# Performance work log

Hardware: AMD Instinct MI355X
Metric: run time of the kernel (lower is better)

The kernel has to match this reference:

```python
import jax, jax.numpy as jnp
import numpy as np

TOP_K = 8


def setup_inputs() -> dict:
    key = jax.random.key(0)
    k1, k2, k3 = jax.random.split(key, 3)
    tokens, hidden, experts = 32768, 2048, 64
    hidden_states = jax.random.normal(k1, (tokens, hidden), dtype=jnp.float32)
    weight = jax.random.normal(k2, (experts, hidden), dtype=jnp.float32) * 0.02
    bias = jax.random.normal(k3, (experts,), dtype=jnp.float32) * 0.02
    return {"hidden_states": hidden_states, "weight": weight, "bias": bias}


def reference(hidden_states, weight, bias):
    # router logits: [tokens, experts]
    logits = jnp.einsum('th,eh->te', hidden_states, weight) + bias
    top_vals, top_idx = jax.lax.top_k(logits, TOP_K)            # [tokens, k]
    top_probs = jax.nn.softmax(top_vals, axis=-1)               # softmax over selected k
    rows = jnp.arange(logits.shape[0])[:, None]                  # [tokens, 1]
    scores = jnp.zeros_like(logits).at[rows, top_idx].set(top_probs)
    return scores, top_idx
```

## Files before the change

### kernel.cpp

```cpp
#include <hip/hip_runtime.h>
#include <math.h>

typedef _Float16 half8 __attribute__((ext_vector_type(8)));
typedef _Float16 half4 __attribute__((ext_vector_type(4)));
typedef float    f32x4 __attribute__((ext_vector_type(4)));

#define TOKENS  32768
#define HIDDEN  2048
#define EXPERTS 64
#define TOPK    8
#define BKW     64
#define NWIN    (HIDDEN / BKW)
#define LDH     72

__global__ __launch_bounds__(256, 1)
void router_mfma(const float* __restrict__ A,
                 const float* __restrict__ W,
                 const float* __restrict__ bias,
                 float* __restrict__ out) {
    __shared__ __align__(16) _Float16 hsm[4 * 64 * LDH];
    _Float16* Ahs = hsm;
    _Float16* Als = hsm + 64 * LDH;
    _Float16* Whs = hsm + 2 * 64 * LDH;
    _Float16* Wls = hsm + 3 * 64 * LDH;

    const int tid = threadIdx.x;
    const int w   = tid >> 6;
    const int l   = tid & 63;
    const int g   = blockIdx.x;

    const int s_tok = tid >> 4;
    const int s_c   = tid & 15;
    const int we = tid >> 2;
    const int wc = tid & 3;

    const float* Abase = A + (size_t)g * 64 * HIDDEN;
    const float* WBase = W + (size_t)we * HIDDEN;

    f32x4 acc[4];
    #pragma unroll
    for (int n = 0; n < 4; ++n) acc[n] = (f32x4){0.f, 0.f, 0.f, 0.f};

    float4 ar0, ar1, ar2, ar3;
    float4 wr0, wr1, wr2, wr3;

    #define LOADA(win) do {                                                  \
        const float* p_ = Abase + (size_t)(win) * BKW + s_c * 4;             \
        ar0 = *(const float4*)(p_ + (size_t)(s_tok     ) * HIDDEN);          \
        ar1 = *(const float4*)(p_ + (size_t)(s_tok + 16) * HIDDEN);          \
        ar2 = *(const float4*)(p_ + (size_t)(s_tok + 32) * HIDDEN);          \
        ar3 = *(const float4*)(p_ + (size_t)(s_tok + 48) * HIDDEN);          \
    } while (0)

    #define LOADW(win) do {                                                  \
        const float* q_ = WBase + (size_t)(win) * BKW + wc * 8;              \
        wr0 = *(const float4*)(q_);                                          \
        wr1 = *(const float4*)(q_ + 4);                                      \
        wr2 = *(const float4*)(q_ + 32);                                     \
        wr3 = *(const float4*)(q_ + 36);                                     \
    } while (0)

    #define SPLIT4(HS, LS, v, OFF) do {                                      \
        _Float16 h0_ = (_Float16)(v).x, h1_ = (_Float16)(v).y;               \
        _Float16 h2_ = (_Float16)(v).z, h3_ = (_Float16)(v).w;               \
        half4 hh_ = {h0_, h1_, h2_, h3_};                                    \
        half4 ll_ = {(_Float16)((v).x - (float)h0_),                         \
                     (_Float16)((v).y - (float)h1_),                         \
                     (_Float16)((v).z - (float)h2_),                         \
                     (_Float16)((v).w - (float)h3_)};                        \
        *(half4*)(&(HS)[(OFF)]) = hh_;                                       \
        *(half4*)(&(LS)[(OFF)]) = ll_;                                       \
    } while (0)

    #define STAGE() do {                                                     \
        SPLIT4(Ahs, Als, ar0, (s_tok     ) * LDH + s_c * 4);                 \
        SPLIT4(Ahs, Als, ar1, (s_tok + 16) * LDH + s_c * 4);                 \
        SPLIT4(Ahs, Als, ar2, (s_tok + 32) * LDH + s_c * 4);                 \
        SPLIT4(Ahs, Als, ar3, (s_tok + 48) * LDH + s_c * 4);                 \
        SPLIT4(Whs, Wls, wr0, we * LDH + wc * 8);                            \
        SPLIT4(Whs, Wls, wr1, we * LDH + wc * 8 + 4);                        \
        SPLIT4(Whs, Wls, wr2, we * LDH + wc * 8 + 32);                       \
        SPLIT4(Whs, Wls, wr3, we * LDH + wc * 8 + 36);                       \
    } while (0)

    LOADA(0);
    LOADW(0);

    #pragma unroll 1
    for (int win = 0; win < NWIN; ++win) {
        __syncthreads();
        STAGE();
        __syncthreads();

        if (win + 1 < NWIN) {
            LOADA(win + 1);
            LOADW(win + 1);
        }

        #pragma unroll
        for (int ks = 0; ks < 2; ++ks) {
            const int ko = ks * 32 + (l >> 4) * 8;
            half8 ahi = *(const half8*)(&Ahs[(w * 16 + (l & 15)) * LDH + ko]);
            half8 alo = *(const half8*)(&Als[(w * 16 + (l & 15)) * LDH + ko]);
            #pragma unroll
            for (int n = 0; n < 4; ++n) {
                half8 bh = *(const half8*)(&Whs[(n * 16 + (l & 15)) * LDH + ko]);
                half8 bl = *(const half8*)(&Wls[(n * 16 + (l & 15)) * LDH + ko]);
                acc[n] = __builtin_amdgcn_mfma_f32_16x16x32_f16(ahi, bh, acc[n], 0, 0, 0);
                acc[n] = __builtin_amdgcn_mfma_f32_16x16x32_f16(ahi, bl, acc[n], 0, 0, 0);
                acc[n] = __builtin_amdgcn_mfma_f32_16x16x32_f16(alo, bh, acc[n], 0, 0, 0);
            }
        }
    }
    #undef LOADA
    #undef LOADW
    #undef SPLIT4
    #undef STAGE

    __syncthreads();
    float* lg = (float*)hsm;
    float* sc = (float*)hsm + 64 * 68;

    #pragma unroll
    for (int n = 0; n < 4; ++n) {
        float b = bias[n * 16 + (l & 15)];
        #pragma unroll
        for (int q = 0; q < 4; ++q) {
            int trow = w * 16 + (l >> 4) * 4 + q;
            lg[trow * 68 + n * 16 + (l & 15)] = acc[n][q] + b;
        }
    }
    for (int i = tid; i < 64 * 65; i += 256) sc[i] = 0.f;
    __syncthreads();

    if (tid < 64) {
        const int t = tid;
        float v[64];
        #pragma unroll
        for (int e = 0; e < 64; ++e) v[e] = lg[t * 68 + e];

        float tvals[TOPK]; int tix[TOPK]; float probs[TOPK];
        unsigned long long chosen = 0ull;
        #pragma unroll
        for (int j = 0; j < TOPK; ++j) {
            float best = -INFINITY; int bi = 0;
            #pragma unroll
            for (int e = 0; e < 64; ++e) {
                bool ok = ((chosen >> e) & 1ull) == 0ull;
                if (ok && v[e] > best) { best = v[e]; bi = e; }
            }
            chosen |= (1ull << bi);
            tvals[j] = best; tix[j] = bi;
        }
        float m = tvals[0];
        float ssum = 0.f;
        #pragma unroll
        for (int j = 0; j < TOPK; ++j) { probs[j] = __expf(tvals[j] - m); ssum += probs[j]; }
        float inv = 1.f / ssum;
        #pragma unroll
        for (int j = 0; j < TOPK; ++j) probs[j] *= inv;

        #pragma unroll
        for (int j = 0; j < TOPK; ++j) sc[t * 65 + tix[j]] = probs[j];

        float* oidx = out + (size_t)TOKENS * EXPERTS;
        const int token = g * 64 + t;
        #pragma unroll
        for (int j = 0; j < TOPK; ++j) oidx[(size_t)token * TOPK + j] = (float)tix[j];
    }
    __syncthreads();

    float* oscore = out + (size_t)g * 4096;
    #pragma unroll
    for (int p = 0; p < 4; ++p) {
        int fi  = tid + 256 * p;
        int tok = fi >> 4;
        int es  = (fi & 15) * 4;
        float4 vv;
        vv.x = sc[tok * 65 + es + 0];
        vv.y = sc[tok * 65 + es + 1];
        vv.z = sc[tok * 65 + es + 2];
        vv.w = sc[tok * 65 + es + 3];
        *(float4*)(oscore + (size_t)fi * 4) = vv;
    }
}

extern "C" void kernel_launch(void* const* d_in, const int* in_sizes, int n_in,
                              void* d_out, int out_size, void* d_ws, size_t ws_size,
                              hipStream_t stream) {
    const float* A    = (const float*)d_in[0];
    const float* W    = (const float*)d_in[1];
    const float* bias = (const float*)d_in[2];
    float* out = (float*)d_out;
    (void)d_ws; (void)ws_size;

    router_mfma<<<TOKENS / 64, 256, 0, stream>>>(A, W, bias, out);
}
```

Baseline: 61.21 us.

## Double-buffer A register prefetch two windows ahead with raw LDS barriers

Keeps two register sets for the activation tile so global loads for window s+2 are issued while window s is staged and computed, deepening the prefetch distance. It also replaces __syncthreads with a raw s_barrier that waits only on LDS counters, so outstanding global loads are not drained at each barrier. The trade is higher register pressure from the extra float4 set, and correctness now depends on the hand-placed waitcnt and sched_barrier ordering.

```diff
diff --git a/kernel.cpp b/kernel.cpp
--- a/kernel.cpp
+++ b/kernel.cpp
@@ -14,10 +14,10 @@
 #define LDH     72
 
 __global__ __launch_bounds__(256, 1)
-void router_mfma(const float* __restrict__ A,
-                 const float* __restrict__ W,
-                 const float* __restrict__ bias,
-                 float* __restrict__ out) {
+void router_p2(const float* __restrict__ A,
+               const float* __restrict__ W,
+               const float* __restrict__ bias,
+               float* __restrict__ out) {
     __shared__ __align__(16) _Float16 hsm[4 * 64 * LDH];
     _Float16* Ahs = hsm;
     _Float16* Als = hsm + 64 * LDH;
@@ -41,15 +41,16 @@
     #pragma unroll
     for (int n = 0; n < 4; ++n) acc[n] = (f32x4){0.f, 0.f, 0.f, 0.f};
 
-    float4 ar0, ar1, ar2, ar3;
+    float4 arA0, arA1, arA2, arA3;
+    float4 arB0, arB1, arB2, arB3;
     float4 wr0, wr1, wr2, wr3;
 
-    #define LOADA(win) do {                                                  \
+    #define LOADA(S, win) do {                                               \
         const float* p_ = Abase + (size_t)(win) * BKW + s_c * 4;             \
-        ar0 = *(const float4*)(p_ + (size_t)(s_tok     ) * HIDDEN);          \
-        ar1 = *(const float4*)(p_ + (size_t)(s_tok + 16) * HIDDEN);          \
-        ar2 = *(const float4*)(p_ + (size_t)(s_tok + 32) * HIDDEN);          \
-        ar3 = *(const float4*)(p_ + (size_t)(s_tok + 48) * HIDDEN);          \
+        ar##S##0 = *(const float4*)(p_ + (size_t)(s_tok     ) * HIDDEN);     \
+        ar##S##1 = *(const float4*)(p_ + (size_t)(s_tok + 16) * HIDDEN);     \
+        ar##S##2 = *(const float4*)(p_ + (size_t)(s_tok + 32) * HIDDEN);     \
+        ar##S##3 = *(const float4*)(p_ + (size_t)(s_tok + 48) * HIDDEN);     \
     } while (0)
 
     #define LOADW(win) do {                                                  \
@@ -72,50 +73,67 @@
         *(half4*)(&(LS)[(OFF)]) = ll_;                                       \
     } while (0)
 
-    #define STAGE() do {                                                     \
-        SPLIT4(Ahs, Als, ar0, (s_tok     ) * LDH + s_c * 4);                 \
-        SPLIT4(Ahs, Als, ar1, (s_tok + 16) * LDH + s_c * 4);                 \
-        SPLIT4(Ahs, Als, ar2, (s_tok + 32) * LDH + s_c * 4);                 \
-        SPLIT4(Ahs, Als, ar3, (s_tok + 48) * LDH + s_c * 4);                 \
+    #define STAGE(S) do {                                                    \
+        SPLIT4(Ahs, Als, ar##S##0, (s_tok     ) * LDH + s_c * 4);            \
+        SPLIT4(Ahs, Als, ar##S##1, (s_tok + 16) * LDH + s_c * 4);            \
+        SPLIT4(Ahs, Als, ar##S##2, (s_tok + 32) * LDH + s_c * 4);            \
+        SPLIT4(Ahs, Als, ar##S##3, (s_tok + 48) * LDH + s_c * 4);            \
         SPLIT4(Whs, Wls, wr0, we * LDH + wc * 8);                            \
         SPLIT4(Whs, Wls, wr1, we * LDH + wc * 8 + 4);                        \
         SPLIT4(Whs, Wls, wr2, we * LDH + wc * 8 + 32);                       \
         SPLIT4(Whs, Wls, wr3, we * LDH + wc * 8 + 36);                       \
     } while (0)
 
-    LOADA(0);
+    #define COMPUTE() do {                                                   \
+        _Pragma("unroll")                                                    \
+        for (int ks = 0; ks < 2; ++ks) {                                     \
+            const int ko = ks * 32 + (l >> 4) * 8;                           \
+            half8 ahi = *(const half8*)(&Ahs[(w * 16 + (l & 15)) * LDH + ko]); \
+            half8 alo = *(const half8*)(&Als[(w * 16 + (l & 15)) * LDH + ko]); \
+            _Pragma("unroll")                                                \
+            for (int n = 0; n < 4; ++n) {                                    \
+                half8 bh = *(const half8*)(&Whs[(n * 16 + (l & 15)) * LDH + ko]); \
+                half8 bl = *(const half8*)(&Wls[(n * 16 + (l & 15)) * LDH + ko]); \
+                acc[n] = __builtin_amdgcn_mfma_f32_16x16x32_f16(ahi, bh, acc[n], 0, 0, 0); \
+                acc[n] = __builtin_amdgcn_mfma_f32_16x16x32_f16(ahi, bl, acc[n], 0, 0, 0); \
+                acc[n] = __builtin_amdgcn_mfma_f32_16x16x32_f16(alo, bh, acc[n], 0, 0, 0); \
+            }                                                                \
+        }                                                                    \
+    } while (0)
+
+    #define BARRAW() do {                                                    \
+        asm volatile("s_waitcnt lgkmcnt(0)" ::: "memory");                   \
+        __builtin_amdgcn_sched_barrier(0);                                   \
+        __builtin_amdgcn_s_barrier();                                        \
+        __builtin_amdgcn_sched_barrier(0);                                   \
+    } while (0)
+
+    LOADA(A, 0);
     LOADW(0);
+    LOADA(B, 1);
 
     #pragma unroll 1
-    for (int win = 0; win < NWIN; ++win) {
-        __syncthreads();
-        STAGE();
-        __syncthreads();
-
-        if (win + 1 < NWIN) {
-            LOADA(win + 1);
-            LOADW(win + 1);
-        }
-
-        #pragma unroll
-        for (int ks = 0; ks < 2; ++ks) {
-            const int ko = ks * 32 + (l >> 4) * 8;
-            half8 ahi = *(const half8*)(&Ahs[(w * 16 + (l & 15)) * LDH + ko]);
-            half8 alo = *(const half8*)(&Als[(w * 16 + (l & 15)) * LDH + ko]);
-            #pragma unroll
-            for (int n = 0; n < 4; ++n) {
-                half8 bh = *(const half8*)(&Whs[(n * 16 + (l & 15)) * LDH + ko]);
-                half8 bl = *(const half8*)(&Wls[(n * 16 + (l & 15)) * LDH + ko]);
-                acc[n] = __builtin_amdgcn_mfma_f32_16x16x32_f16(ahi, bh, acc[n], 0, 0, 0);
-                acc[n] = __builtin_amdgcn_mfma_f32_16x16x32_f16(ahi, bl, acc[n], 0, 0, 0);
-                acc[n] = __builtin_amdgcn_mfma_f32_16x16x32_f16(alo, bh, acc[n], 0, 0, 0);
-            }
-        }
+    for (int s = 0; s < NWIN; s += 2) {
+        BARRAW();
+        STAGE(A);
+        if (s + 1 < NWIN) LOADW(s + 1);
+        if (s + 2 < NWIN) LOADA(A, s + 2);
+        BARRAW();
+        COMPUTE();
+
+        BARRAW();
+        STAGE(B);
+        if (s + 2 < NWIN) LOADW(s + 2);
+        if (s + 3 < NWIN) LOADA(B, s + 3);
+        BARRAW();
+        COMPUTE();
     }
     #undef LOADA
     #undef LOADW
     #undef SPLIT4
     #undef STAGE
+    #undef COMPUTE
+    #undef BARRAW
 
     __syncthreads();
     float* lg = (float*)hsm;
@@ -194,5 +212,5 @@
     float* out = (float*)d_out;
     (void)d_ws; (void)ws_size;
 
-    router_mfma<<<TOKENS / 64, 256, 0, stream>>>(A, W, bias, out);
+    router_p2<<<TOKENS / 64, 256, 0, stream>>>(A, W, bias, out);
 }
```

Result: slower. 62.58 us (+2.2%).
